# Kernel tuning notes

Hardware: AMD Instinct MI355X
Metric: run time of the kernel (lower is better)

Reference implementation:

```python
import jax, jax.numpy as jnp
import numpy as np
import math

B, S, D, H, KVH = 4, 2048, 4096, 32, 8
HD = D // H          # 128
N_REP = H // KVH     # 4
MAX_S = 2048


def setup_inputs() -> dict:
    key = jax.random.key(0)
    ks = jax.random.split(key, 6)
    x = jax.random.normal(ks[0], (B, S, D), dtype=jnp.float32)
    sc = 0.02
    wq = jax.random.normal(ks[1], (D, H * HD), dtype=jnp.float32) * sc
    wk = jax.random.normal(ks[2], (D, KVH * HD), dtype=jnp.float32) * sc
    wv = jax.random.normal(ks[3], (D, KVH * HD), dtype=jnp.float32) * sc
    wo = jax.random.normal(ks[4], (H * HD, D), dtype=jnp.float32) * sc
    # RoPE tables (matches llama precompute_freqs_cis, theta=10000)
    inv_freq = 1.0 / (10000.0 ** (np.arange(0, HD, 2, dtype=np.float32) / HD))  # [HD/2]
    t = np.arange(S, dtype=np.float32)
    freqs = np.outer(t, inv_freq)  # [S, HD/2]
    cos = jnp.asarray(np.cos(freqs), dtype=jnp.float32)
    sin = jnp.asarray(np.sin(freqs), dtype=jnp.float32)
    cache_k = jnp.zeros((B, MAX_S, KVH, HD), dtype=jnp.float32)
    cache_v = jnp.zeros((B, MAX_S, KVH, HD), dtype=jnp.float32)
    return {"x": x, "wq": wq, "wk": wk, "wv": wv, "wo": wo,
            "cos": cos, "sin": sin, "cache_k": cache_k, "cache_v": cache_v,
            "start_pos": 0}


def _apply_rope(x, cos, sin):
    # x: [B, S, h, HD]; interleaved complex rotation, as torch view_as_complex
    xr = x.reshape(*x.shape[:-1], HD // 2, 2)
    x0, x1 = xr[..., 0], xr[..., 1]
    c = cos[None, :, None, :]
    s = sin[None, :, None, :]
    o0 = x0 * c - x1 * s
    o1 = x0 * s + x1 * c
    return jnp.stack([o0, o1], axis=-1).reshape(x.shape)


def reference(x, wq, wk, wv, wo, cos, sin, cache_k, cache_v, start_pos):
    bsz, seqlen, _ = x.shape
    xq = (x @ wq).reshape(bsz, seqlen, H, HD)
    xk = (x @ wk).reshape(bsz, seqlen, KVH, HD)
    xv = (x @ wv).reshape(bsz, seqlen, KVH, HD)
    xq = _apply_rope(xq, cos, sin)
    xk = _apply_rope(xk, cos, sin)
    # KV cache update then slice [:start_pos+seqlen]
    cache_k = jax.lax.dynamic_update_slice(cache_k, xk, (0, start_pos, 0, 0))
    cache_v = jax.lax.dynamic_update_slice(cache_v, xv, (0, start_pos, 0, 0))
    kv_len = start_pos + seqlen
    keys = cache_k[:, :kv_len]    # [B, K, KVH, HD]
    values = cache_v[:, :kv_len]
    # repeat_kv: expand kv heads by n_rep (GQA)
    keys = jnp.repeat(keys, N_REP, axis=2)      # [B, K, H, HD]
    values = jnp.repeat(values, N_REP, axis=2)
    scores = jnp.einsum('bqhd,bkhd->bhqk', xq, keys) / math.sqrt(HD)
    probs = jax.nn.softmax(scores.astype(jnp.float32), axis=-1).astype(xq.dtype)
    out = jnp.einsum('bhqk,bkhd->bqhd', probs, values)
    out = out.reshape(bsz, seqlen, H * HD)
    return out @ wo
```

## Files before the change

kernel.cpp:

```cpp
#include <hip/hip_runtime.h>
#include <math.h>
#include <stdint.h>

typedef unsigned short u16;
typedef __attribute__((ext_vector_type(8))) short short8;
typedef __attribute__((ext_vector_type(4))) float f32x4;

#define B_   4
#define S_   2048
#define D_   4096
#define H_   32
#define KVH_ 8
#define HD_  128
#define NQKV 6144
#define MTOT 8192
#define ATT_SCALE 0.08838834764831845f
#define QSCL (ATT_SCALE * 1.4426950408889634f)
#define DEFER_L2 11.541560327111707f

__device__ __forceinline__ float bf2f(u16 u) {
  unsigned x = ((unsigned)u) << 16;
  return __builtin_bit_cast(float, x);
}
__device__ __forceinline__ u16 f2bf(float f) {
  unsigned x = __builtin_bit_cast(unsigned, f);
  x += 0x7fffu + ((x >> 16) & 1u);
  return (u16)(x >> 16);
}
__device__ __forceinline__ unsigned pack2bf(float a, float b) {
  return (unsigned)f2bf(a) | ((unsigned)f2bf(b) << 16);
}
__device__ __forceinline__ float exp2_hw(float x) {
  float r;
  asm("v_exp_f32 %0, %1" : "=v"(r) : "v"(x));
  return r;
}

typedef const __attribute__((address_space(1))) void* gas1p;
typedef __attribute__((address_space(3))) void* las3p;
__device__ __forceinline__ void gload16(const void* g, void* l) {
  __builtin_amdgcn_global_load_lds((gas1p)g, (las3p)l, 16, 0, 0);
}

__device__ __forceinline__ int swz64(int row, int kc) {
  return row * 64 + ((kc ^ (row & 7)) << 3);
}
__device__ __forceinline__ int swz128(int row, int kc) {
  return row * 128 + ((kc ^ (row & 7)) << 3);
}

__global__ void cast_f32_to_bf16(const float* __restrict__ in, u16* __restrict__ out, long n) {
  long i = ((long)blockIdx.x * 256 + threadIdx.x) * 4;
  if (i >= n) return;
  float4 v = *(const float4*)(in + i);
  ushort4 o;
  o.x = f2bf(v.x); o.y = f2bf(v.y); o.z = f2bf(v.z); o.w = f2bf(v.w);
  *(ushort4*)(out + i) = o;
}

__global__ void transpose_cast(const float* __restrict__ in, u16* __restrict__ out, int K, int N) {
  __shared__ u16 tile[32][33];
  int n0 = blockIdx.x * 32, k0 = blockIdx.y * 32;
  int tx = threadIdx.x, ty = threadIdx.y;
  for (int i = ty; i < 32; i += 8)
    tile[i][tx] = f2bf(in[(long)(k0 + i) * N + n0 + tx]);
  __syncthreads();
  for (int i = ty; i < 32; i += 8)
    out[(long)(n0 + i) * K + k0 + tx] = tile[tx][i];
}

template <int OUTF32>
__global__ __launch_bounds__(512, 2) void gemm256(const u16* __restrict__ A,
                                                  const u16* __restrict__ BT,
                                                  void* __restrict__ Cout,
                                                  int M, int N, int K) {
  __shared__ u16 Ls[2][2][2][128 * 64];
  int tid = threadIdx.x, lane = tid & 63, wid = tid >> 6;
  int wm = wid >> 2, wn = wid & 3;
  int m0 = blockIdx.y * 256, n0 = blockIdx.x * 256;
  int frow = lane & 15, fk = lane >> 4;

  f32x4 acc[8][4];
#pragma unroll
  for (int i = 0; i < 8; i++)
#pragma unroll
    for (int j = 0; j < 4; j++) acc[i][j] = (f32x4){0.f, 0.f, 0.f, 0.f};

  int srow = lane >> 3;
  int sc = ((lane & 7) ^ srow) * 8;
  const u16* a0 = A + (long)(m0 + (2 * wid + 0) * 8 + srow) * K + sc;
  const u16* a1 = A + (long)(m0 + (2 * wid + 1) * 8 + srow) * K + sc;
  const u16* b0 = BT + (long)(n0 + (2 * wid + 0) * 8 + srow) * K + sc;
  const u16* b1 = BT + (long)(n0 + (2 * wid + 1) * 8 + srow) * K + sc;
  long hstep = (long)128 * K;

#define STAGE_A(buf, half, t) do {                                              \
    gload16(a0 + (half) * hstep + (long)(t) * 64, &Ls[buf][0][half][(2 * wid + 0) * 512]); \
    gload16(a1 + (half) * hstep + (long)(t) * 64, &Ls[buf][0][half][(2 * wid + 1) * 512]); \
  } while (0)
#define STAGE_B(buf, half, t) do {                                              \
    gload16(b0 + (half) * hstep + (long)(t) * 64, &Ls[buf][1][half][(2 * wid + 0) * 512]); \
    gload16(b1 + (half) * hstep + (long)(t) * 64, &Ls[buf][1][half][(2 * wid + 1) * 512]); \
  } while (0)

  int nk = K / 64;
  STAGE_A(0, 0, 0); STAGE_A(0, 1, 0); STAGE_B(0, 0, 0); STAGE_B(0, 1, 0);
  STAGE_B(1, 0, 1); STAGE_B(1, 1, 1);
  asm volatile("s_waitcnt vmcnt(4)" ::: "memory");
  __builtin_amdgcn_s_barrier();

#define PHASE(P, STAGE_STMT, VM_STMT)                                           \
  {                                                                             \
    short8 af[2][2];                                                            \
    _Pragma("unroll") for (int mm = 0; mm < 2; mm++)                            \
      _Pragma("unroll") for (int kk = 0; kk < 2; kk++)                          \
        af[mm][kk] = *(const short8*)&Ah[swz64((2 * (P) + mm) * 16 + frow, kk * 4 + fk)]; \
    STAGE_STMT;                                                                 \
    VM_STMT;                                                                    \
    __builtin_amdgcn_s_barrier();                                               \
    asm volatile("s_waitcnt lgkmcnt(0)" ::: "memory");                          \
    __builtin_amdgcn_sched_barrier(0);                                          \
    __builtin_amdgcn_s_setprio(1);                                              \
    _Pragma("unroll") for (int mm = 0; mm < 2; mm++)                            \
      _Pragma("unroll") for (int n = 0; n < 4; n++)                             \
        _Pragma("unroll") for (int kk = 0; kk < 2; kk++)                        \
          acc[2 * (P) + mm][n] = __builtin_amdgcn_mfma_f32_16x16x32_bf16(       \
              af[mm][kk], bfr[n][kk], acc[2 * (P) + mm][n], 0, 0, 0);           \
    __builtin_amdgcn_s_setprio(0);                                              \
    __builtin_amdgcn_s_barrier();                                               \
  }

  for (int t = 0; t < nk; ++t) {
    int pi = t & 1;
    const u16* Ah = &Ls[pi][0][wm][0];
    const u16* Bh = &Ls[pi][1][wn >> 1][0];
    int brow = (wn & 1) * 64;
    short8 bfr[4][2];
#pragma unroll
    for (int n = 0; n < 4; n++)
#pragma unroll
      for (int kk = 0; kk < 2; kk++)
        bfr[n][kk] = *(const short8*)&Bh[swz64(brow + n * 16 + frow, kk * 4 + fk)];

    PHASE(0, if (t + 1 < nk) STAGE_A(pi ^ 1, 0, t + 1), );
    PHASE(1, if (t + 1 < nk) STAGE_A(pi ^ 1, 1, t + 1), );
    PHASE(2, if (t + 2 < nk) STAGE_B(pi, 0, t + 2), );
    PHASE(3, if (t + 2 < nk) STAGE_B(pi, 1, t + 2),
          if (t + 2 < nk) { asm volatile("s_waitcnt vmcnt(4)" ::: "memory"); }
          else            { asm volatile("s_waitcnt vmcnt(0)" ::: "memory"); });
  }
#undef PHASE
#undef STAGE_A
#undef STAGE_B

  int cc = lane & 15, cr = fk * 4;
#pragma unroll
  for (int i = 0; i < 8; i++)
#pragma unroll
    for (int j = 0; j < 4; j++)
#pragma unroll
      for (int r = 0; r < 4; r++) {
        int m = m0 + wm * 128 + i * 16 + cr + r;
        int n = n0 + wn * 64 + j * 16 + cc;
        if (OUTF32)
          ((float*)Cout)[(long)m * N + n] = acc[i][j][r];
        else
          ((u16*)Cout)[(long)m * N + n] = f2bf(acc[i][j][r]);
      }
}

__global__ void rope_k_kernel(u16* __restrict__ qkv, const float* __restrict__ cosb,
                              const float* __restrict__ sinb, const int* __restrict__ start_pos) {
  long tid = (long)blockIdx.x * 256 + threadIdx.x;
  const long total = (long)MTOT * 512;
  if (tid >= total) return;
  int row = (int)(tid >> 9);
  int p = (int)(tid & 511);
  int col = D_ + p * 2;
  int i = p & 63;
  int s = row & (S_ - 1);
  int pos = s + *start_pos;
  float c = cosb[pos * 64 + i];
  float sn = sinb[pos * 64 + i];
  u16* ptr = qkv + (long)row * NQKV + col;
  unsigned v = *(unsigned*)ptr;
  float x0 = bf2f((u16)(v & 0xffff));
  float x1 = bf2f((u16)(v >> 16));
  float o0 = x0 * c - x1 * sn;
  float o1 = x0 * sn + x1 * c;
  *(unsigned*)ptr = pack2bf(o0, o1);
}

__global__ void build_vt(const u16* __restrict__ qkv, u16* __restrict__ vt) {
  int bk = blockIdx.z;
  int b = bk >> 3, kvh = bk & 7;
  int s0 = blockIdx.x * 32, d0 = blockIdx.y * 32;
  __shared__ u16 tile[32][33];
  int tx = threadIdx.x, ty = threadIdx.y;
  const u16* src = qkv + (long)(b * S_) * NQKV + D_ + KVH_ * HD_ + kvh * HD_;
  for (int i = ty; i < 32; i += 8)
    tile[i][tx] = src[(long)(s0 + i) * NQKV + d0 + tx];
  __syncthreads();
  u16* dst = vt + ((long)(b * KVH_ + kvh) * HD_) * S_;
  for (int i = ty; i < 32; i += 8)
    dst[(long)(d0 + i) * S_ + s0 + tx] = tile[tx][i];
}

__global__ __launch_bounds__(512, 1) void attn_kernel(const u16* __restrict__ qkv,
                                                      const u16* __restrict__ vt,
                                                      u16* __restrict__ obuf,
                                                      const float* __restrict__ cosb,
                                                      const float* __restrict__ sinb,
                                                      const int* __restrict__ start_pos) {
  int nb = gridDim.x;
  int fid = (int)((blockIdx.x & 7) * (nb >> 3) + (blockIdx.x >> 3));
  int bx = fid & 7;
  int bh = fid >> 3;
  int b = bh >> 5, h = bh & 31;
  int kvh = h >> 2;
  int q0 = bx * 256;
  int tid = threadIdx.x, lane = tid & 63, wid = tid >> 6;

  __shared__ u16 Ks[2][64 * 128];
  __shared__ u16 VTs[2][128 * 64];
  __shared__ u16 Ps[8][32 * 64];

  int frow = lane & 15;
  int fk = lane >> 4;

  short8 qf[2][4];
#pragma unroll
  for (int qq = 0; qq < 2; ++qq) {
    int s = q0 + wid * 32 + qq * 16 + frow;
    int pos = s + *start_pos;
    const float* cb = cosb + pos * 64;
    const float* sb = sinb + pos * 64;
    const u16* qbase = qkv + (long)(b * S_ + s) * NQKV + h * HD_;
#pragma unroll
    for (int kd = 0; kd < 4; ++kd) {
      short8 v = *(const short8*)(qbase + kd * 32 + fk * 8);
      union { short8 s8; unsigned u[4]; } w;
#pragma unroll
      for (int j = 0; j < 4; ++j) {
        int i = kd * 16 + fk * 4 + j;
        float c = cb[i], sn = sb[i];
        float x0 = bf2f((u16)v[2 * j]), x1 = bf2f((u16)v[2 * j + 1]);
        w.u[j] = pack2bf((x0 * c - x1 * sn) * QSCL, (x0 * sn + x1 * c) * QSCL);
      }
      qf[qq][kd] = w.s8;
    }
  }

  f32x4 acc_o[2][8];
#pragma unroll
  for (int qq = 0; qq < 2; qq++)
#pragma unroll
    for (int i = 0; i < 8; i++) acc_o[qq][i] = (f32x4){0.f, 0.f, 0.f, 0.f};
  float m_r[2] = {-1e30f, -1e30f};
  float l_r[2] = {0.f, 0.f};

  const u16* kgl[2];
  const u16* vgl[2];
#pragma unroll
  for (int j = 0; j < 2; j++) {
    int gk = j * 8 + wid;
    int rk = gk * 4 + (lane >> 4);
    int ck = (lane & 15) ^ (rk & 7);
    kgl[j] = qkv + (long)(b * S_ + rk) * NQKV + D_ + kvh * HD_ + ck * 8;
    int gv = j * 8 + wid;
    int rv = gv * 8 + (lane >> 3);
    int cv = (lane & 7) ^ (rv & 7);
    vgl[j] = vt + ((long)(b * KVH_ + kvh) * HD_ + rv) * S_ + cv * 8;
  }

#define STAGE_KV(buf, t) do {                                                   \
    _Pragma("unroll") for (int j = 0; j < 2; j++) {                             \
      int g = j * 8 + wid;                                                      \
      gload16(kgl[j] + (long)((t) * 64) * NQKV, &Ks[buf][g * 512]);             \
      gload16(vgl[j] + (t) * 64, &VTs[buf][g * 512]);                           \
    }                                                                           \
  } while (0)

  auto COMPUTE = [&](const u16* Kb, const u16* Vb) {
    f32x4 sc[4][2];
#pragma unroll
    for (int f = 0; f < 4; f++)
#pragma unroll
      for (int qq = 0; qq < 2; qq++) sc[f][qq] = (f32x4){0.f, 0.f, 0.f, 0.f};
#pragma unroll
    for (int f = 0; f < 4; f++)
#pragma unroll
      for (int kd = 0; kd < 4; kd++) {
        short8 kf = *(const short8*)&Kb[swz128(f * 16 + frow, kd * 4 + fk)];
        sc[f][0] = __builtin_amdgcn_mfma_f32_16x16x32_bf16(kf, qf[0][kd], sc[f][0], 0, 0, 0);
        sc[f][1] = __builtin_amdgcn_mfma_f32_16x16x32_bf16(kf, qf[1][kd], sc[f][1], 0, 0, 0);
      }

    float mx[2];
#pragma unroll
    for (int qq = 0; qq < 2; ++qq) {
      float mf[4];
#pragma unroll
      for (int f = 0; f < 4; f++)
        mf[f] = fmaxf(fmaxf(fmaxf(sc[f][qq][0], sc[f][qq][1]), sc[f][qq][2]), sc[f][qq][3]);
      float m = fmaxf(fmaxf(fmaxf(mf[0], mf[1]), mf[2]), mf[3]);
      m = fmaxf(m, __shfl_xor(m, 16, 64));
      m = fmaxf(m, __shfl_xor(m, 32, 64));
      mx[qq] = m;
    }
    if (!__all((mx[0] <= m_r[0] + DEFER_L2) && (mx[1] <= m_r[1] + DEFER_L2))) {
#pragma unroll
      for (int qq = 0; qq < 2; ++qq) {
        float mnew = fmaxf(m_r[qq], mx[qq]);
        float scl = exp2_hw(m_r[qq] - mnew);
        l_r[qq] *= scl;
        m_r[qq] = mnew;
#pragma unroll
        for (int df = 0; df < 8; df++) acc_o[qq][df] *= scl;
      }
    }

#pragma unroll
    for (int qq = 0; qq < 2; ++qq) {
      float nm = m_r[qq];
      float rs = 0.f;
      int prow = qq * 16 + frow;
      int pbase = prow * 64 + (fk & 1) * 4;
      int q7 = frow & 7;
#pragma unroll
      for (int f = 0; f < 4; f++) {
        float p0 = exp2_hw(sc[f][qq][0] - nm);
        float p1 = exp2_hw(sc[f][qq][1] - nm);
        float p2 = exp2_hw(sc[f][qq][2] - nm);
        float p3 = exp2_hw(sc[f][qq][3] - nm);
        rs += (p0 + p1) + (p2 + p3);
        int chunk = (f * 2 + (fk >> 1)) ^ q7;
        uint2 wv2; wv2.x = pack2bf(p0, p1); wv2.y = pack2bf(p2, p3);
        *(uint2*)&Ps[wid][pbase + (chunk << 3)] = wv2;
      }
      l_r[qq] += rs;
    }

    asm volatile("s_waitcnt lgkmcnt(0)" ::: "memory");
    __builtin_amdgcn_sched_barrier(0);

    short8 pf[2][2];
#pragma unroll
    for (int qq = 0; qq < 2; qq++)
#pragma unroll
      for (int kk = 0; kk < 2; kk++)
        pf[qq][kk] = *(const short8*)&Ps[wid][(qq * 16 + frow) * 64 + (((kk * 4 + fk) ^ (frow & 7)) << 3)];
#pragma unroll
    for (int df = 0; df < 8; df++)
#pragma unroll
      for (int kk = 0; kk < 2; kk++) {
        short8 vf = *(const short8*)&Vb[swz64(df * 16 + frow, kk * 4 + fk)];
        acc_o[0][df] = __builtin_amdgcn_mfma_f32_16x16x32_bf16(vf, pf[0][kk], acc_o[0][df], 0, 0, 0);
        acc_o[1][df] = __builtin_amdgcn_mfma_f32_16x16x32_bf16(vf, pf[1][kk], acc_o[1][df], 0, 0, 0);
      }
    __syncthreads();
  };

  const int ntiles = S_ / 64;
  STAGE_KV(0, 0);
  for (int tt = 0; tt < ntiles; tt += 2) {
    STAGE_KV(1, tt + 1);
    asm volatile("s_waitcnt vmcnt(4)" ::: "memory");
    __builtin_amdgcn_s_barrier();
    __builtin_amdgcn_sched_barrier(0);
    COMPUTE(&Ks[0][0], &VTs[0][0]);
    if (tt + 2 < ntiles) {
      STAGE_KV(0, tt + 2);
      asm volatile("s_waitcnt vmcnt(4)" ::: "memory");
    } else {
      asm volatile("s_waitcnt vmcnt(0)" ::: "memory");
    }
    __builtin_amdgcn_s_barrier();
    __builtin_amdgcn_sched_barrier(0);
    COMPUTE(&Ks[1][0], &VTs[1][0]);
  }
#undef STAGE_KV

#pragma unroll
  for (int qq = 0; qq < 2; ++qq) {
    float lv = l_r[qq];
    lv += __shfl_xor(lv, 16, 64);
    lv += __shfl_xor(lv, 32, 64);
    float inv = 1.0f / lv;
    long srow = (long)(b * S_ + q0 + wid * 32 + qq * 16 + frow);
    u16* orow = obuf + srow * D_ + h * HD_ + fk * 4;
#pragma unroll
    for (int df = 0; df < 8; df++) {
      uint2 ov;
      ov.x = pack2bf(acc_o[qq][df][0] * inv, acc_o[qq][df][1] * inv);
      ov.y = pack2bf(acc_o[qq][df][2] * inv, acc_o[qq][df][3] * inv);
      *(uint2*)(orow + df * 16) = ov;
    }
  }
}

extern "C" void kernel_launch(void* const* d_in, const int* in_sizes, int n_in,
                              void* d_out, int out_size, void* d_ws, size_t ws_size,
                              hipStream_t stream) {
  const float* x = (const float*)d_in[0];
  const float* wq = (const float*)d_in[1];
  const float* wk = (const float*)d_in[2];
  const float* wv = (const float*)d_in[3];
  const float* wo = (const float*)d_in[4];
  const float* cosb = (const float*)d_in[5];
  const float* sinb = (const float*)d_in[6];
  const int* start_pos = (const int*)d_in[9];
  float* out = (float*)d_out;

  char* ws = (char*)d_ws;
  u16* xb = (u16*)ws;
  u16* wqkvT = (u16*)(ws + 67108864L);
  u16* woT = (u16*)(ws + 117440512L);
  u16* qkvb = (u16*)(ws + 150994944L);
  u16* vtb = (u16*)(ws + 251658240L);
  u16* obuf = xb;

  cast_f32_to_bf16<<<dim3(32768), dim3(256), 0, stream>>>(x, xb, (long)MTOT * D_);

  transpose_cast<<<dim3(128, 128), dim3(32, 8), 0, stream>>>(wq, wqkvT, D_, 4096);
  transpose_cast<<<dim3(32, 128), dim3(32, 8), 0, stream>>>(wk, wqkvT + (long)4096 * D_, D_, 1024);
  transpose_cast<<<dim3(32, 128), dim3(32, 8), 0, stream>>>(wv, wqkvT + (long)5120 * D_, D_, 1024);
  transpose_cast<<<dim3(128, 128), dim3(32, 8), 0, stream>>>(wo, woT, D_, 4096);

  gemm256<0><<<dim3(NQKV / 256, MTOT / 256), dim3(512), 0, stream>>>(xb, wqkvT, qkvb, MTOT, NQKV, D_);

  rope_k_kernel<<<dim3(16384), dim3(256), 0, stream>>>(qkvb, cosb, sinb, start_pos);

  build_vt<<<dim3(64, 4, 32), dim3(32, 8), 0, stream>>>(qkvb, vtb);

  attn_kernel<<<dim3(1024), dim3(512), 0, stream>>>(qkvb, vtb, obuf, cosb, sinb, start_pos);

  gemm256<1><<<dim3(D_ / 256, MTOT / 256), dim3(512), 0, stream>>>(obuf, woT, out, MTOT, D_, D_);
}
```

Baseline: 1.025 ms.

## Remap GEMM blocks per XCD, halve attention P scratch, raise attention occupancy

The GEMM launches become one-dimensional, and block IDs are remapped so that consecutive tiles land on the same XCD. The goal is better L2 reuse of A and B tiles across the chiplets. The attention kernel now stages the probability tile one 16-row half at a time through a halved per-wave LDS buffer, which cuts LDS use. Its launch bounds rise to 2 blocks per CU to allow higher occupancy. The cost is register pressure that may cause spills, plus extra serialization between the two P halves.

```diff
diff --git a/kernel.cpp b/kernel.cpp
--- a/kernel.cpp
+++ b/kernel.cpp
@@ -77,7 +77,10 @@
   __shared__ u16 Ls[2][2][2][128 * 64];
   int tid = threadIdx.x, lane = tid & 63, wid = tid >> 6;
   int wm = wid >> 2, wn = wid & 3;
-  int m0 = blockIdx.y * 256, n0 = blockIdx.x * 256;
+  int nbg = gridDim.x;
+  int fidg = (int)((blockIdx.x & 7) * (nbg >> 3) + (blockIdx.x >> 3));
+  int gx = N >> 8;
+  int m0 = (fidg / gx) << 8, n0 = (fidg % gx) << 8;
   int frow = lane & 15, fk = lane >> 4;
 
   f32x4 acc[8][4];
@@ -206,7 +209,7 @@
     dst[(long)(d0 + i) * S_ + s0 + tx] = tile[tx][i];
 }
 
-__global__ __launch_bounds__(512, 1) void attn_kernel(const u16* __restrict__ qkv,
+__global__ __launch_bounds__(512, 2) void attn_kernel(const u16* __restrict__ qkv,
                                                       const u16* __restrict__ vt,
                                                       u16* __restrict__ obuf,
                                                       const float* __restrict__ cosb,
@@ -223,7 +226,7 @@
 
   __shared__ u16 Ks[2][64 * 128];
   __shared__ u16 VTs[2][128 * 64];
-  __shared__ u16 Ps[8][32 * 64];
+  __shared__ u16 Ps[8][16 * 64];
 
   int frow = lane & 15;
   int fk = lane >> 4;
@@ -281,6 +284,8 @@
     }                                                                           \
   } while (0)
 
+  u16* Php = &Ps[wid][0];
+
   auto COMPUTE = [&](const u16* Kb, const u16* Vb) {
     f32x4 sc[4][2];
 #pragma unroll
@@ -320,43 +325,63 @@
       }
     }
 
-#pragma unroll
-    for (int qq = 0; qq < 2; ++qq) {
-      float nm = m_r[qq];
+    int pbase = frow * 64 + (fk & 1) * 4;
+    int q7 = frow & 7;
+    short8 pf0[2], pf1[2];
+
+    {
+      float nm = m_r[0];
       float rs = 0.f;
-      int prow = qq * 16 + frow;
-      int pbase = prow * 64 + (fk & 1) * 4;
-      int q7 = frow & 7;
 #pragma unroll
       for (int f = 0; f < 4; f++) {
-        float p0 = exp2_hw(sc[f][qq][0] - nm);
-        float p1 = exp2_hw(sc[f][qq][1] - nm);
-        float p2 = exp2_hw(sc[f][qq][2] - nm);
-        float p3 = exp2_hw(sc[f][qq][3] - nm);
+        float p0 = exp2_hw(sc[f][0][0] - nm);
+        float p1 = exp2_hw(sc[f][0][1] - nm);
+        float p2 = exp2_hw(sc[f][0][2] - nm);
+        float p3 = exp2_hw(sc[f][0][3] - nm);
         rs += (p0 + p1) + (p2 + p3);
         int chunk = (f * 2 + (fk >> 1)) ^ q7;
         uint2 wv2; wv2.x = pack2bf(p0, p1); wv2.y = pack2bf(p2, p3);
-        *(uint2*)&Ps[wid][pbase + (chunk << 3)] = wv2;
-      }
-      l_r[qq] += rs;
-    }
-
+        *(uint2*)&Php[pbase + (chunk << 3)] = wv2;
+      }
+      l_r[0] += rs;
+    }
+    __builtin_amdgcn_sched_barrier(0);
+#pragma unroll
+    for (int kk = 0; kk < 2; kk++)
+      pf0[kk] = *(const short8*)&Php[frow * 64 + (((kk * 4 + fk) ^ q7) << 3)];
     asm volatile("s_waitcnt lgkmcnt(0)" ::: "memory");
     __builtin_amdgcn_sched_barrier(0);
 
-    short8 pf[2][2];
-#pragma unroll
-    for (int qq = 0; qq < 2; qq++)
-#pragma unroll
-      for (int kk = 0; kk < 2; kk++)
-        pf[qq][kk] = *(const short8*)&Ps[wid][(qq * 16 + frow) * 64 + (((kk * 4 + fk) ^ (frow & 7)) << 3)];
+    {
+      float nm = m_r[1];
+      float rs = 0.f;
+#pragma unroll
+      for (int f = 0; f < 4; f++) {
+        float p0 = exp2_hw(sc[f][1][0] - nm);
+        float p1 = exp2_hw(sc[f][1][1] - nm);
+        float p2 = exp2_hw(sc[f][1][2] - nm);
+        float p3 = exp2_hw(sc[f][1][3] - nm);
+        rs += (p0 + p1) + (p2 + p3);
+        int chunk = (f * 2 + (fk >> 1)) ^ q7;
+        uint2 wv2; wv2.x = pack2bf(p0, p1); wv2.y = pack2bf(p2, p3);
+        *(uint2*)&Php[pbase + (chunk << 3)] = wv2;
+      }
+      l_r[1] += rs;
+    }
+    __builtin_amdgcn_sched_barrier(0);
+#pragma unroll
+    for (int kk = 0; kk < 2; kk++)
+      pf1[kk] = *(const short8*)&Php[frow * 64 + (((kk * 4 + fk) ^ q7) << 3)];
+    asm volatile("s_waitcnt lgkmcnt(0)" ::: "memory");
+    __builtin_amdgcn_sched_barrier(0);
+
 #pragma unroll
     for (int df = 0; df < 8; df++)
 #pragma unroll
       for (int kk = 0; kk < 2; kk++) {
         short8 vf = *(const short8*)&Vb[swz64(df * 16 + frow, kk * 4 + fk)];
-        acc_o[0][df] = __builtin_amdgcn_mfma_f32_16x16x32_bf16(vf, pf[0][kk], acc_o[0][df], 0, 0, 0);
-        acc_o[1][df] = __builtin_amdgcn_mfma_f32_16x16x32_bf16(vf, pf[1][kk], acc_o[1][df], 0, 0, 0);
+        acc_o[0][df] = __builtin_amdgcn_mfma_f32_16x16x32_bf16(vf, pf0[kk], acc_o[0][df], 0, 0, 0);
+        acc_o[1][df] = __builtin_amdgcn_mfma_f32_16x16x32_bf16(vf, pf1[kk], acc_o[1][df], 0, 0, 0);
       }
     __syncthreads();
   };
@@ -427,7 +452,7 @@
   transpose_cast<<<dim3(32, 128), dim3(32, 8), 0, stream>>>(wv, wqkvT + (long)5120 * D_, D_, 1024);
   transpose_cast<<<dim3(128, 128), dim3(32, 8), 0, stream>>>(wo, woT, D_, 4096);
 
-  gemm256<0><<<dim3(NQKV / 256, MTOT / 256), dim3(512), 0, stream>>>(xb, wqkvT, qkvb, MTOT, NQKV, D_);
+  gemm256<0><<<dim3((NQKV / 256) * (MTOT / 256)), dim3(512), 0, stream>>>(xb, wqkvT, qkvb, MTOT, NQKV, D_);
 
   rope_k_kernel<<<dim3(16384), dim3(256), 0, stream>>>(qkvb, cosb, sinb, start_pos);
 
@@ -435,5 +460,5 @@
 
   attn_kernel<<<dim3(1024), dim3(512), 0, stream>>>(qkvb, vtb, obuf, cosb, sinb, start_pos);
 
-  gemm256<1><<<dim3(D_ / 256, MTOT / 256), dim3(512), 0, stream>>>(obuf, woT, out, MTOT, D_, D_);
-}
+  gemm256<1><<<dim3((D_ / 256) * (MTOT / 256)), dim3(512), 0, stream>>>(obuf, woT, out, MTOT, D_, D_);
+}
```

Measured after the change: 1.049 ms. 2.3% more time.
